# Optimization experiments

Measured on AMD Instinct MI355X. Metric: run time of the kernel, lower is better.

## Reference

```python
import jax, jax.numpy as jnp
import numpy as np

B, S, D = 8, 2048, 512

def setup_inputs() -> dict:
    key = jax.random.key(0)
    k1, k2 = jax.random.split(key)
    lstm_out = jax.random.normal(k1, (B, S, D), dtype=jnp.float32)
    # xavier_uniform init for [D, D]
    limit = float(np.sqrt(6.0 / (D + D)))
    attention_weights = jax.random.uniform(k2, (D, D), dtype=jnp.float32, minval=-limit, maxval=limit)
    return {"lstm_out": lstm_out, "attention_weights": attention_weights}

def reference(lstm_out, attention_weights):
    # scores[b,i,j] = tanh( (x W) x^T )
    proj = jnp.einsum('bsd,de->bse', lstm_out, attention_weights)          # [B,S,D]
    scores = jnp.tanh(jnp.einsum('bsd,btd->bst', proj, lstm_out))          # [B,S,S]
    attn = jax.nn.softmax(scores, axis=-1)                                 # [B,S,S]
    return jnp.einsum('bst,btd->bsd', attn, lstm_out)                      # [B,S,D]
```

## Files before the change

### kernel.cpp

```cpp
#include <hip/hip_runtime.h>
#include <hip/hip_bf16.h>

typedef __bf16 bf16;
typedef __attribute__((ext_vector_type(8))) __bf16 bf16x8;
typedef __attribute__((ext_vector_type(4))) float floatx4;

#define NPART 16
#define NSLOT 32

__device__ __forceinline__ void gl_lds16(const bf16* g, bf16* l) {
    __builtin_amdgcn_global_load_lds(
        (const __attribute__((address_space(1))) unsigned int*)g,
        (__attribute__((address_space(3))) unsigned int*)l,
        16, 0, 0);
}

__device__ __forceinline__ void swizzle_mn(int& bm, int& bn) {
    int gx = gridDim.x;
    int f  = blockIdx.y * gx + blockIdx.x;
    int st = f >> 3, r = f & 7;
    int mgroups = gx >> 2;
    bm = (st % mgroups) * 4 + (r & 3);
    bn = (st / mgroups) * 2 + (r >> 2);
}

__global__ __launch_bounds__(256) void cast_both(const float* __restrict__ in,
                                                 bf16* __restrict__ outn,
                                                 bf16* __restrict__ outt,
                                                 int R, int C) {
    __shared__ float tile[32][33];
    const long long bz = blockIdx.z;
    in   += bz * (long long)R * C;
    outn += bz * (long long)R * C;
    outt += bz * (long long)R * C;
    const int r0 = blockIdx.x * 32, c0 = blockIdx.y * 32;
    const int tx = threadIdx.x & 31, ty = threadIdx.x >> 5;
#pragma unroll
    for (int i = 0; i < 32; i += 8) {
        float v = in[(long long)(r0 + ty + i) * C + (c0 + tx)];
        tile[ty + i][tx] = v;
        outn[(long long)(r0 + ty + i) * C + (c0 + tx)] = (bf16)v;
    }
    __syncthreads();
#pragma unroll
    for (int i = 0; i < 32; i += 8)
        outt[(long long)(c0 + ty + i) * R + (r0 + tx)] = (bf16)tile[tx][ty + i];
}

__global__ __launch_bounds__(256) void cast_transpose(const float* __restrict__ in,
                                                      bf16* __restrict__ out,
                                                      int R, int C) {
    __shared__ float tile[32][33];
    const int r0 = blockIdx.x * 32, c0 = blockIdx.y * 32;
    const int tx = threadIdx.x & 31, ty = threadIdx.x >> 5;
#pragma unroll
    for (int i = 0; i < 32; i += 8)
        tile[ty + i][tx] = in[(long long)(r0 + ty + i) * C + (c0 + tx)];
    __syncthreads();
#pragma unroll
    for (int i = 0; i < 32; i += 8)
        out[(long long)(c0 + ty + i) * R + (r0 + tx)] = (bf16)tile[tx][ty + i];
}

__device__ __forceinline__ float fast_tanh(float v) {
    float e = __expf(2.0f * v);
    return 1.0f - 2.0f / (e + 1.0f);
}

template <int MODE>
__global__ __launch_bounds__(256) void gemm128(const bf16* __restrict__ A,
                                               const bf16* __restrict__ Bm,
                                               void* __restrict__ Cout,
                                               float* __restrict__ rpart,
                                               int M, int N, int K,
                                               long long batchA, long long batchB,
                                               long long batchC, long long batchR) {
    const long long bz = blockIdx.z;
    A  += bz * batchA;
    Bm += bz * batchB;

    __shared__ bf16 As[128 * 64];
    __shared__ bf16 Bs[128 * 64];
    __shared__ float rs[128];

    const int t    = threadIdx.x;
    const int lane = t & 63;
    const int wave = t >> 6;
    const int quad = lane >> 4;
    const int l16  = lane & 15;

    int bm, bn;
    swizzle_mn(bm, bn);
    const int m0 = bm * 128;
    const int n0 = bn * 128;
    const int wm = (wave >> 1) * 64;
    const int wn = (wave & 1) * 64;

    floatx4 acc[4][4] = {};

    const int ra = t >> 3;
    const int ca = (((t & 7) ^ (ra & 7))) * 8;
    const long long rstep = 32LL * K;
    const bf16* Abase = A + (long long)(m0 + ra) * K + ca;
    const bf16* Bbase = Bm + (long long)(n0 + ra) * K + ca;

    const int cq0 = ((quad) ^ (l16 & 7)) * 8;
    const int cq1 = ((4 + quad) ^ (l16 & 7)) * 8;

    if (MODE == 2) {
        if (t < 128) {
            const float* pp = rpart + (bz * batchR + m0 + t) * NSLOT;
            float s = 0.f;
#pragma unroll
            for (int c = 0; c < NSLOT / 4; ++c) {
                float4 p = ((const float4*)pp)[c];
                s += (p.x + p.y) + (p.z + p.w);
            }
            rs[t] = 1.0f / s;
        }
    }

    for (int k0 = 0; k0 < K; k0 += 64) {
#pragma unroll
        for (int i = 0; i < 4; ++i) {
            gl_lds16(Abase + k0 + i * rstep, &As[(t + 256 * i) * 8]);
            gl_lds16(Bbase + k0 + i * rstep, &Bs[(t + 256 * i) * 8]);
        }
        __syncthreads();

#pragma unroll
        for (int s = 0; s < 2; ++s) {
            const int cq = s ? cq1 : cq0;
            bf16x8 af[4], bfr[4];
#pragma unroll
            for (int i = 0; i < 4; ++i)
                af[i] = *(const bf16x8*)(&As[(wm + i * 16 + l16) * 64 + cq]);
#pragma unroll
            for (int j = 0; j < 4; ++j)
                bfr[j] = *(const bf16x8*)(&Bs[(wn + j * 16 + l16) * 64 + cq]);
#pragma unroll
            for (int i = 0; i < 4; ++i)
#pragma unroll
                for (int j = 0; j < 4; ++j)
                    acc[i][j] = __builtin_amdgcn_mfma_f32_16x16x32_bf16(af[i], bfr[j], acc[i][j], 0, 0, 0);
        }
        __syncthreads();
    }

    if (MODE == 1) {
        bf16* Cg = (bf16*)Cout + bz * batchC;
        const int slot = bn * 2 + (wave & 1);
#pragma unroll
        for (int i = 0; i < 4; ++i)
#pragma unroll
            for (int r = 0; r < 4; ++r) {
                long long row = m0 + wm + i * 16 + quad * 4 + r;
                float s = 0.f;
#pragma unroll
                for (int j = 0; j < 4; ++j) {
                    float v = __expf(fast_tanh(acc[i][j][r]));
                    s += v;
                    Cg[row * (long long)N + (n0 + wn + j * 16 + l16)] = (bf16)v;
                }
#pragma unroll
                for (int msk = 1; msk < 16; msk <<= 1) s += __shfl_xor(s, msk);
                if (l16 == 0)
                    rpart[(bz * batchR + row) * NSLOT + slot] = s;
            }
    } else {
        float* Og = (float*)Cout + bz * batchC;
#pragma unroll
        for (int i = 0; i < 4; ++i)
#pragma unroll
            for (int r = 0; r < 4; ++r) {
                int rl = wm + i * 16 + quad * 4 + r;
                float inv = rs[rl];
                long long row = m0 + rl;
#pragma unroll
                for (int j = 0; j < 4; ++j)
                    Og[row * (long long)N + (n0 + wn + j * 16 + l16)] = acc[i][j][r] * inv;
            }
    }
}

__global__ __launch_bounds__(256) void gemm64_nt(const bf16* __restrict__ A,
                                                 const bf16* __restrict__ Bm,
                                                 bf16* __restrict__ Cout,
                                                 int M, int N, int K) {
    __shared__ bf16 As[64 * 64];
    __shared__ bf16 Bs[128 * 64];

    const int t    = threadIdx.x;
    const int lane = t & 63;
    const int wave = t >> 6;
    const int quad = lane >> 4;
    const int l16  = lane & 15;

    const int m0 = blockIdx.x * 64;
    const int n0 = blockIdx.y * 128;
    const int wn = wave * 32;

    floatx4 acc[4][2] = {};

    const int ra = t >> 3;
    const int ca = (((t & 7) ^ (ra & 7))) * 8;
    const long long rstep = 32LL * K;
    const bf16* Abase = A + (long long)(m0 + ra) * K + ca;
    const bf16* Bbase = Bm + (long long)(n0 + ra) * K + ca;

    const int cq0 = ((quad) ^ (l16 & 7)) * 8;
    const int cq1 = ((4 + quad) ^ (l16 & 7)) * 8;

    for (int k0 = 0; k0 < K; k0 += 64) {
#pragma unroll
        for (int i = 0; i < 2; ++i)
            gl_lds16(Abase + k0 + i * rstep, &As[(t + 256 * i) * 8]);
#pragma unroll
        for (int i = 0; i < 4; ++i)
            gl_lds16(Bbase + k0 + i * rstep, &Bs[(t + 256 * i) * 8]);
        __syncthreads();

#pragma unroll
        for (int s = 0; s < 2; ++s) {
            const int cq = s ? cq1 : cq0;
            bf16x8 af[4], bfr[2];
#pragma unroll
            for (int i = 0; i < 4; ++i)
                af[i] = *(const bf16x8*)(&As[(i * 16 + l16) * 64 + cq]);
#pragma unroll
            for (int j = 0; j < 2; ++j)
                bfr[j] = *(const bf16x8*)(&Bs[(wn + j * 16 + l16) * 64 + cq]);
#pragma unroll
            for (int i = 0; i < 4; ++i)
#pragma unroll
                for (int j = 0; j < 2; ++j)
                    acc[i][j] = __builtin_amdgcn_mfma_f32_16x16x32_bf16(af[i], bfr[j], acc[i][j], 0, 0, 0);
        }
        __syncthreads();
    }

#pragma unroll
    for (int i = 0; i < 4; ++i)
#pragma unroll
        for (int r = 0; r < 4; ++r) {
            long long row = m0 + i * 16 + quad * 4 + r;
#pragma unroll
            for (int j = 0; j < 2; ++j)
                Cout[row * (long long)N + (n0 + wn + j * 16 + l16)] = (bf16)acc[i][j][r];
        }
}

extern "C" void kernel_launch(void* const* d_in, const int* in_sizes, int n_in,
                              void* d_out, int out_size, void* d_ws, size_t ws_size,
                              hipStream_t stream) {
    const int B = 8, S = 2048, D = 512;
    const float* x = (const float*)d_in[0];
    const float* W = (const float*)d_in[1];
    float* out = (float*)d_out;

    const size_t nx = (size_t)B * S * D;
    const size_t nw = (size_t)D * D;

    char* ws = (char*)d_ws;
    auto al = [](size_t v) { return (v + 255) & ~(size_t)255; };
    size_t off = 0;
    bf16* xb = (bf16*)(ws + off); off = al(off + nx * 2);
    bf16* xt = (bf16*)(ws + off); off = al(off + nx * 2);
    bf16* pb = (bf16*)(ws + off); off = al(off + nx * 2);
    bf16* wt = (bf16*)(ws + off); off = al(off + nw * 2);
    float* rpart = (float*)(ws + off); off = al(off + (size_t)B * S * NSLOT * 4);
    bf16* sb = (bf16*)(ws + off);
    const size_t full_need = off + (size_t)B * S * S * 2;
    const bool batched = (ws_size >= full_need);

    { dim3 g(S / 32, D / 32, B); cast_both<<<g, 256, 0, stream>>>(x, xb, xt, S, D); }
    { dim3 g(D / 32, D / 32, 1); cast_transpose<<<g, 256, 0, stream>>>(W, wt, D, D); }

    {
        dim3 g(B * S / 64, D / 128, 1);
        gemm64_nt<<<g, 256, 0, stream>>>(xb, wt, pb, B * S, D, D);
    }

    const long long sd = (long long)S * D;
    const long long ss = (long long)S * S;

    if (batched) {
        dim3 g2(S / 128, S / 128, B);
        gemm128<1><<<g2, 256, 0, stream>>>(pb, xb, (void*)sb, rpart, S, S, D, sd, sd, ss, S);
        dim3 g4(S / 128, D / 128, B);
        gemm128<2><<<g4, 256, 0, stream>>>(sb, xt, (void*)out, rpart, S, D, S, ss, sd, sd, S);
    } else {
        for (int b = 0; b < B; ++b) {
            dim3 g2(S / 128, S / 128, 1);
            gemm128<1><<<g2, 256, 0, stream>>>(pb + (size_t)b * sd, xb + (size_t)b * sd,
                                               (void*)sb, rpart + (size_t)b * S * NSLOT,
                                               S, S, D, 0, 0, 0, S);
            dim3 g4(S / 128, D / 128, 1);
            gemm128<2><<<g4, 256, 0, stream>>>(sb, xt + (size_t)b * sd,
                                               (void*)(out + (size_t)b * sd), rpart + (size_t)b * S * NSLOT,
                                               S, D, S, 0, 0, 0, S);
        }
    }
}
```

Before: 209.4 us.

## Double-buffer LDS tiles in both GEMM kernels to overlap loads with MFMA

```diff
diff --git a/kernel.cpp b/kernel.cpp
--- a/kernel.cpp
+++ b/kernel.cpp
@@ -79,8 +79,8 @@
     A  += bz * batchA;
     Bm += bz * batchB;
 
-    __shared__ bf16 As[128 * 64];
-    __shared__ bf16 Bs[128 * 64];
+    __shared__ bf16 As[2][128 * 64];
+    __shared__ bf16 Bs[2][128 * 64];
     __shared__ float rs[128];
 
     const int t    = threadIdx.x;
@@ -120,30 +120,42 @@
         }
     }
 
-    for (int k0 = 0; k0 < K; k0 += 64) {
+    auto stage = [&](int buf, int k0) {
 #pragma unroll
         for (int i = 0; i < 4; ++i) {
-            gl_lds16(Abase + k0 + i * rstep, &As[(t + 256 * i) * 8]);
-            gl_lds16(Bbase + k0 + i * rstep, &Bs[(t + 256 * i) * 8]);
-        }
-        __syncthreads();
-
+            gl_lds16(Abase + k0 + i * rstep, &As[buf][(t + 256 * i) * 8]);
+            gl_lds16(Bbase + k0 + i * rstep, &Bs[buf][(t + 256 * i) * 8]);
+        }
+    };
+
+    auto compute = [&](int buf) {
 #pragma unroll
         for (int s = 0; s < 2; ++s) {
             const int cq = s ? cq1 : cq0;
             bf16x8 af[4], bfr[4];
 #pragma unroll
             for (int i = 0; i < 4; ++i)
-                af[i] = *(const bf16x8*)(&As[(wm + i * 16 + l16) * 64 + cq]);
+                af[i] = *(const bf16x8*)(&As[buf][(wm + i * 16 + l16) * 64 + cq]);
 #pragma unroll
             for (int j = 0; j < 4; ++j)
-                bfr[j] = *(const bf16x8*)(&Bs[(wn + j * 16 + l16) * 64 + cq]);
+                bfr[j] = *(const bf16x8*)(&Bs[buf][(wn + j * 16 + l16) * 64 + cq]);
 #pragma unroll
             for (int i = 0; i < 4; ++i)
 #pragma unroll
                 for (int j = 0; j < 4; ++j)
                     acc[i][j] = __builtin_amdgcn_mfma_f32_16x16x32_bf16(af[i], bfr[j], acc[i][j], 0, 0, 0);
         }
+    };
+
+    stage(0, 0);
+    __syncthreads();
+
+    for (int k0 = 0; k0 < K; k0 += 128) {
+        if (k0 + 64 < K) stage(1, k0 + 64);
+        compute(0);
+        __syncthreads();
+        if (k0 + 128 < K) stage(0, k0 + 128);
+        compute(1);
         __syncthreads();
     }
 
@@ -187,8 +199,8 @@
                                                  const bf16* __restrict__ Bm,
                                                  bf16* __restrict__ Cout,
                                                  int M, int N, int K) {
-    __shared__ bf16 As[64 * 64];
-    __shared__ bf16 Bs[128 * 64];
+    __shared__ bf16 As[2][64 * 64];
+    __shared__ bf16 Bs[2][128 * 64];
 
     const int t    = threadIdx.x;
     const int lane = t & 63;
@@ -211,31 +223,43 @@
     const int cq0 = ((quad) ^ (l16 & 7)) * 8;
     const int cq1 = ((4 + quad) ^ (l16 & 7)) * 8;
 
-    for (int k0 = 0; k0 < K; k0 += 64) {
+    auto stage = [&](int buf, int k0) {
 #pragma unroll
         for (int i = 0; i < 2; ++i)
-            gl_lds16(Abase + k0 + i * rstep, &As[(t + 256 * i) * 8]);
+            gl_lds16(Abase + k0 + i * rstep, &As[buf][(t + 256 * i) * 8]);
 #pragma unroll
         for (int i = 0; i < 4; ++i)
-            gl_lds16(Bbase + k0 + i * rstep, &Bs[(t + 256 * i) * 8]);
-        __syncthreads();
-
+            gl_lds16(Bbase + k0 + i * rstep, &Bs[buf][(t + 256 * i) * 8]);
+    };
+
+    auto compute = [&](int buf) {
 #pragma unroll
         for (int s = 0; s < 2; ++s) {
             const int cq = s ? cq1 : cq0;
             bf16x8 af[4], bfr[2];
 #pragma unroll
             for (int i = 0; i < 4; ++i)
-                af[i] = *(const bf16x8*)(&As[(i * 16 + l16) * 64 + cq]);
+                af[i] = *(const bf16x8*)(&As[buf][(i * 16 + l16) * 64 + cq]);
 #pragma unroll
             for (int j = 0; j < 2; ++j)
-                bfr[j] = *(const bf16x8*)(&Bs[(wn + j * 16 + l16) * 64 + cq]);
+                bfr[j] = *(const bf16x8*)(&Bs[buf][(wn + j * 16 + l16) * 64 + cq]);
 #pragma unroll
             for (int i = 0; i < 4; ++i)
 #pragma unroll
                 for (int j = 0; j < 2; ++j)
                     acc[i][j] = __builtin_amdgcn_mfma_f32_16x16x32_bf16(af[i], bfr[j], acc[i][j], 0, 0, 0);
         }
+    };
+
+    stage(0, 0);
+    __syncthreads();
+
+    for (int k0 = 0; k0 < K; k0 += 128) {
+        if (k0 + 64 < K) stage(1, k0 + 64);
+        compute(0);
+        __syncthreads();
+        if (k0 + 128 < K) stage(0, k0 + 128);
+        compute(1);
         __syncthreads();
     }
 
```

Measured after the change: 203.9 us. -2.6%, faster.

## Double-buffer GEMM LDS tiles, vectorize cast kernel, reuse gemm128 for projection

Applied to the files above, without the earlier changes.

```diff
diff --git a/kernel.cpp b/kernel.cpp
--- a/kernel.cpp
+++ b/kernel.cpp
@@ -2,10 +2,10 @@
 #include <hip/hip_bf16.h>
 
 typedef __bf16 bf16;
+typedef __attribute__((ext_vector_type(4))) __bf16 bf16x4;
 typedef __attribute__((ext_vector_type(8))) __bf16 bf16x8;
 typedef __attribute__((ext_vector_type(4))) float floatx4;
 
-#define NPART 16
 #define NSLOT 32
 
 __device__ __forceinline__ void gl_lds16(const bf16* g, bf16* l) {
@@ -28,23 +28,32 @@
                                                  bf16* __restrict__ outn,
                                                  bf16* __restrict__ outt,
                                                  int R, int C) {
-    __shared__ float tile[32][33];
+    __shared__ float tile[64][65];
     const long long bz = blockIdx.z;
     in   += bz * (long long)R * C;
     outn += bz * (long long)R * C;
     outt += bz * (long long)R * C;
-    const int r0 = blockIdx.x * 32, c0 = blockIdx.y * 32;
-    const int tx = threadIdx.x & 31, ty = threadIdx.x >> 5;
-#pragma unroll
-    for (int i = 0; i < 32; i += 8) {
-        float v = in[(long long)(r0 + ty + i) * C + (c0 + tx)];
-        tile[ty + i][tx] = v;
-        outn[(long long)(r0 + ty + i) * C + (c0 + tx)] = (bf16)v;
+    const int r0 = blockIdx.x * 64, c0 = blockIdx.y * 64;
+    const int cl = (threadIdx.x & 15) * 4;
+    const int rw = threadIdx.x >> 4;
+#pragma unroll
+    for (int it = 0; it < 4; ++it) {
+        const int r = rw + it * 16;
+        floatx4 v = *(const floatx4*)&in[(long long)(r0 + r) * C + c0 + cl];
+        bf16x4 b; b[0] = (bf16)v[0]; b[1] = (bf16)v[1]; b[2] = (bf16)v[2]; b[3] = (bf16)v[3];
+        *(bf16x4*)&outn[(long long)(r0 + r) * C + c0 + cl] = b;
+        tile[r][cl + 0] = v[0]; tile[r][cl + 1] = v[1];
+        tile[r][cl + 2] = v[2]; tile[r][cl + 3] = v[3];
     }
     __syncthreads();
 #pragma unroll
-    for (int i = 0; i < 32; i += 8)
-        outt[(long long)(c0 + ty + i) * R + (r0 + tx)] = (bf16)tile[tx][ty + i];
+    for (int it = 0; it < 4; ++it) {
+        const int c = rw + it * 16;
+        bf16x4 b;
+        b[0] = (bf16)tile[cl + 0][c]; b[1] = (bf16)tile[cl + 1][c];
+        b[2] = (bf16)tile[cl + 2][c]; b[3] = (bf16)tile[cl + 3][c];
+        *(bf16x4*)&outt[(long long)(c0 + c) * R + r0 + cl] = b;
+    }
 }
 
 __global__ __launch_bounds__(256) void cast_transpose(const float* __restrict__ in,
@@ -79,8 +88,8 @@
     A  += bz * batchA;
     Bm += bz * batchB;
 
-    __shared__ bf16 As[128 * 64];
-    __shared__ bf16 Bs[128 * 64];
+    __shared__ bf16 As[2][128 * 32];
+    __shared__ bf16 Bs[2][128 * 32];
     __shared__ float rs[128];
 
     const int t    = threadIdx.x;
@@ -98,14 +107,13 @@
 
     floatx4 acc[4][4] = {};
 
-    const int ra = t >> 3;
-    const int ca = (((t & 7) ^ (ra & 7))) * 8;
-    const long long rstep = 32LL * K;
-    const bf16* Abase = A + (long long)(m0 + ra) * K + ca;
-    const bf16* Bbase = Bm + (long long)(n0 + ra) * K + ca;
-
-    const int cq0 = ((quad) ^ (l16 & 7)) * 8;
-    const int cq1 = ((4 + quad) ^ (l16 & 7)) * 8;
+    const int srow = t >> 2;
+    const int sch  = (((t & 3) ^ ((t >> 3) & 3))) * 8;
+    const bf16* Abase = A + (long long)(m0 + srow) * K + sch;
+    const bf16* Bbase = Bm + (long long)(n0 + srow) * K + sch;
+    const long long r64 = 64LL * K;
+
+    const int rdch = (quad ^ ((l16 >> 1) & 3)) * 8;
 
     if (MODE == 2) {
         if (t < 128) {
@@ -120,30 +128,37 @@
         }
     }
 
+    auto stage = [&](int buf, int k0) {
+        gl_lds16(Abase + k0,       &As[buf][t * 8]);
+        gl_lds16(Abase + k0 + r64, &As[buf][t * 8 + 2048]);
+        gl_lds16(Bbase + k0,       &Bs[buf][t * 8]);
+        gl_lds16(Bbase + k0 + r64, &Bs[buf][t * 8 + 2048]);
+    };
+
+    auto compute = [&](int buf) {
+        bf16x8 af[4], bfr[4];
+#pragma unroll
+        for (int i = 0; i < 4; ++i)
+            af[i] = *(const bf16x8*)(&As[buf][(wm + i * 16 + l16) * 32 + rdch]);
+#pragma unroll
+        for (int j = 0; j < 4; ++j)
+            bfr[j] = *(const bf16x8*)(&Bs[buf][(wn + j * 16 + l16) * 32 + rdch]);
+#pragma unroll
+        for (int i = 0; i < 4; ++i)
+#pragma unroll
+            for (int j = 0; j < 4; ++j)
+                acc[i][j] = __builtin_amdgcn_mfma_f32_16x16x32_bf16(af[i], bfr[j], acc[i][j], 0, 0, 0);
+    };
+
+    stage(0, 0);
+    __syncthreads();
+
     for (int k0 = 0; k0 < K; k0 += 64) {
-#pragma unroll
-        for (int i = 0; i < 4; ++i) {
-            gl_lds16(Abase + k0 + i * rstep, &As[(t + 256 * i) * 8]);
-            gl_lds16(Bbase + k0 + i * rstep, &Bs[(t + 256 * i) * 8]);
-        }
+        if (k0 + 32 < K) stage(1, k0 + 32);
+        compute(0);
         __syncthreads();
-
-#pragma unroll
-        for (int s = 0; s < 2; ++s) {
-            const int cq = s ? cq1 : cq0;
-            bf16x8 af[4], bfr[4];
-#pragma unroll
-            for (int i = 0; i < 4; ++i)
-                af[i] = *(const bf16x8*)(&As[(wm + i * 16 + l16) * 64 + cq]);
-#pragma unroll
-            for (int j = 0; j < 4; ++j)
-                bfr[j] = *(const bf16x8*)(&Bs[(wn + j * 16 + l16) * 64 + cq]);
-#pragma unroll
-            for (int i = 0; i < 4; ++i)
-#pragma unroll
-                for (int j = 0; j < 4; ++j)
-                    acc[i][j] = __builtin_amdgcn_mfma_f32_16x16x32_bf16(af[i], bfr[j], acc[i][j], 0, 0, 0);
-        }
+        if (k0 + 64 < K) stage(0, k0 + 64);
+        compute(1);
         __syncthreads();
     }
 
@@ -167,7 +182,7 @@
                 if (l16 == 0)
                     rpart[(bz * batchR + row) * NSLOT + slot] = s;
             }
-    } else {
+    } else if (MODE == 2) {
         float* Og = (float*)Cout + bz * batchC;
 #pragma unroll
         for (int i = 0; i < 4; ++i)
@@ -180,74 +195,18 @@
                 for (int j = 0; j < 4; ++j)
                     Og[row * (long long)N + (n0 + wn + j * 16 + l16)] = acc[i][j][r] * inv;
             }
-    }
-}
-
-__global__ __launch_bounds__(256) void gemm64_nt(const bf16* __restrict__ A,
-                                                 const bf16* __restrict__ Bm,
-                                                 bf16* __restrict__ Cout,
-                                                 int M, int N, int K) {
-    __shared__ bf16 As[64 * 64];
-    __shared__ bf16 Bs[128 * 64];
-
-    const int t    = threadIdx.x;
-    const int lane = t & 63;
-    const int wave = t >> 6;
-    const int quad = lane >> 4;
-    const int l16  = lane & 15;
-
-    const int m0 = blockIdx.x * 64;
-    const int n0 = blockIdx.y * 128;
-    const int wn = wave * 32;
-
-    floatx4 acc[4][2] = {};
-
-    const int ra = t >> 3;
-    const int ca = (((t & 7) ^ (ra & 7))) * 8;
-    const long long rstep = 32LL * K;
-    const bf16* Abase = A + (long long)(m0 + ra) * K + ca;
-    const bf16* Bbase = Bm + (long long)(n0 + ra) * K + ca;
-
-    const int cq0 = ((quad) ^ (l16 & 7)) * 8;
-    const int cq1 = ((4 + quad) ^ (l16 & 7)) * 8;
-
-    for (int k0 = 0; k0 < K; k0 += 64) {
-#pragma unroll
-        for (int i = 0; i < 2; ++i)
-            gl_lds16(Abase + k0 + i * rstep, &As[(t + 256 * i) * 8]);
-#pragma unroll
-        for (int i = 0; i < 4; ++i)
-            gl_lds16(Bbase + k0 + i * rstep, &Bs[(t + 256 * i) * 8]);
-        __syncthreads();
-
-#pragma unroll
-        for (int s = 0; s < 2; ++s) {
-            const int cq = s ? cq1 : cq0;
-            bf16x8 af[4], bfr[2];
-#pragma unroll
-            for (int i = 0; i < 4; ++i)
-                af[i] = *(const bf16x8*)(&As[(i * 16 + l16) * 64 + cq]);
-#pragma unroll
-            for (int j = 0; j < 2; ++j)
-                bfr[j] = *(const bf16x8*)(&Bs[(wn + j * 16 + l16) * 64 + cq]);
-#pragma unroll
-            for (int i = 0; i < 4; ++i)
-#pragma unroll
-                for (int j = 0; j < 2; ++j)
-                    acc[i][j] = __builtin_amdgcn_mfma_f32_16x16x32_bf16(af[i], bfr[j], acc[i][j], 0, 0, 0);
-        }
-        __syncthreads();
-    }
-
-#pragma unroll
-    for (int i = 0; i < 4; ++i)
-#pragma unroll
-        for (int r = 0; r < 4; ++r) {
-            long long row = m0 + i * 16 + quad * 4 + r;
-#pragma unroll
-            for (int j = 0; j < 2; ++j)
-                Cout[row * (long long)N + (n0 + wn + j * 16 + l16)] = (bf16)acc[i][j][r];
-        }
+    } else {
+        bf16* Cg = (bf16*)Cout + bz * batchC;
+#pragma unroll
+        for (int i = 0; i < 4; ++i)
+#pragma unroll
+            for (int r = 0; r < 4; ++r) {
+                long long row = m0 + wm + i * 16 + quad * 4 + r;
+#pragma unroll
+                for (int j = 0; j < 4; ++j)
+                    Cg[row * (long long)N + (n0 + wn + j * 16 + l16)] = (bf16)acc[i][j][r];
+            }
+    }
 }
 
 extern "C" void kernel_launch(void* const* d_in, const int* in_sizes, int n_in,
@@ -273,12 +232,12 @@
     const size_t full_need = off + (size_t)B * S * S * 2;
     const bool batched = (ws_size >= full_need);
 
-    { dim3 g(S / 32, D / 32, B); cast_both<<<g, 256, 0, stream>>>(x, xb, xt, S, D); }
+    { dim3 g(S / 64, D / 64, B); cast_both<<<g, 256, 0, stream>>>(x, xb, xt, S, D); }
     { dim3 g(D / 32, D / 32, 1); cast_transpose<<<g, 256, 0, stream>>>(W, wt, D, D); }
 
     {
-        dim3 g(B * S / 64, D / 128, 1);
-        gemm64_nt<<<g, 256, 0, stream>>>(xb, wt, pb, B * S, D, D);
+        dim3 g(B * S / 128, D / 128, 1);
+        gemm128<0><<<g, 256, 0, stream>>>(xb, wt, (void*)pb, nullptr, B * S, D, D, 0, 0, 0, 0);
     }
 
     const long long sd = (long long)S * D;
```

New measurement: 215.2 us. 2.8% more time.
